# Optimization experiments

Measured on AMD Instinct MI355X. Metric: run time of the kernel, lower is better.

Reference implementation:

```python
import jax, jax.numpy as jnp
import numpy as np

B, L, H, E, F, C = 8, 8192, 512, 8, 1024, 2  # batch, seq, hidden, experts, ffn, capacity factor


def setup_inputs() -> dict:
    key = jax.random.key(0)
    ks = jax.random.split(key, 4)
    x = jax.random.normal(ks[0], (B, L, H), jnp.float32)
    Wg = jax.random.normal(ks[1], (H, E), jnp.float32) * (H ** -0.5)   # gate (no bias)
    W1 = jax.random.normal(ks[2], (E, H, F), jnp.float32) * (H ** -0.5)
    b1 = jnp.zeros((E, F), jnp.float32)
    W2 = jax.random.normal(ks[3], (E, F, H), jnp.float32) * (F ** -0.5)
    b2 = jnp.zeros((E, H), jnp.float32)
    return {"x": x, "Wg": Wg, "W1": W1, "b1": b1, "W2": W2, "b2": b2}


def reference(x, Wg, W1, b1, W2, b2):
    b, l, h = x.shape
    e = Wg.shape[1]
    k = min(max(int(l * C / e), 1), l)  # expert-choice capacity per expert
    # Gate scores: softmax over experts per token, then each expert picks its top-k tokens.
    S = jax.nn.softmax(x @ Wg, axis=-1)          # (b, l, E)
    St = jnp.swapaxes(S, 1, 2)                   # (b, E, l)
    G, I = jax.lax.top_k(St, k)                  # (b, E, k) scores / token indices
    # Dispatch: gather each expert's chosen tokens.
    ex = jnp.take_along_axis(x[:, None], I[..., None], axis=2)   # (b, E, k, h)
    # Grouped expert MLP (Linear -> GELU -> Linear), batched over experts.
    hmid = jax.nn.gelu(jnp.einsum('bekh,ehf->bekf', ex, W1) + b1[None, :, None, :],
                       approximate=False)
    out = jnp.einsum('bekf,efh->bekh', hmid, W2) + b2[None, :, None, :]
    vals = G[..., None] * out                    # weight by gate score
    # Combine: scatter-add expert outputs back to token positions.
    new_x = jnp.zeros_like(x).at[jnp.arange(b)[:, None, None], I].add(vals)
    return new_x
```

## Files before the change

kernel.cpp:

```cpp
#include <hip/hip_runtime.h>
#include <hip/hip_bf16.h>
#include <hip/hip_fp16.h>

typedef float f32x4 __attribute__((ext_vector_type(4)));
typedef _Float16 f16x8 __attribute__((ext_vector_type(8)));
typedef unsigned int u32x4 __attribute__((ext_vector_type(4)));

static constexpr int Bb = 8, Ll = 8192, Hh = 512, Ee = 8, Ff = 1024, KK = 2048;

static __device__ __forceinline__ float fast_rcp(float x) {
#if __has_builtin(__builtin_amdgcn_rcpf)
  return __builtin_amdgcn_rcpf(x);
#else
  return 1.0f / x;
#endif
}

static __device__ __forceinline__ float gelu_exact(float v) {
  float a = __builtin_fabsf(v) * 0.70710678118654752f;
  float t = fast_rcp(__builtin_fmaf(0.47047f, a, 1.0f));
  float p = __builtin_fmaf(0.7478556f, t, -0.0958798f);
  p = __builtin_fmaf(p, t, 0.3480242f);
  p = p * t;
  float e = __expf(-a * a);
  float er = __builtin_fmaf(-p, e, 1.0f);
  er = __builtin_copysignf(er, v);
  return 0.5f * v * (1.0f + er);
}

static __device__ __forceinline__ void nt_store16(const f16x8& v, _Float16* p) {
  __builtin_nontemporal_store(*reinterpret_cast<const u32x4*>(&v),
                              reinterpret_cast<u32x4*>(p));
}

__global__ __launch_bounds__(256) void transpose_cvt_kernel(const float* __restrict__ src,
                                                            _Float16* __restrict__ dst,
                                                            int R, int C) {
  __shared__ float tile[32][33];
  int z = blockIdx.z;
  const float* s = src + (size_t)z * R * C;
  _Float16* d = dst + (size_t)z * R * C;
  int c0 = blockIdx.x * 32, r0 = blockIdx.y * 32;
  int tx = threadIdx.x, ty = threadIdx.y;
#pragma unroll
  for (int i = ty; i < 32; i += 8) tile[i][tx] = s[(size_t)(r0 + i) * C + (c0 + tx)];
  __syncthreads();
#pragma unroll
  for (int i = ty; i < 32; i += 8) d[(size_t)(c0 + i) * R + (r0 + tx)] = (_Float16)tile[tx][i];
}

__global__ __launch_bounds__(256) void gatecvt_kernel(const float* __restrict__ x,
                                                      const float* __restrict__ Wg,
                                                      double* __restrict__ St,
                                                      _Float16* __restrict__ xb) {
  __shared__ float wgt[8][516];
  __shared__ float xs[32][132];
  int tid = threadIdx.x;
  for (int i = tid; i < Hh * Ee; i += 256) wgt[i & 7][i >> 3] = Wg[i];
  int row = tid >> 3, seg = tid & 7;
  int token0 = blockIdx.x * 32;
  const float* xrow = x + (size_t)(token0 + row) * Hh;
  _Float16* xbrow = xb + (size_t)(token0 + row) * Hh;
  float4 r0 = reinterpret_cast<const float4*>(xrow)[seg * 4 + 0];
  float4 r1 = reinterpret_cast<const float4*>(xrow)[seg * 4 + 1];
  float4 r2 = reinterpret_cast<const float4*>(xrow)[seg * 4 + 2];
  float4 r3 = reinterpret_cast<const float4*>(xrow)[seg * 4 + 3];
  double a0 = 0.0, a1 = 0.0, a2 = 0.0, a3 = 0.0;
  for (int c = 0; c < 4; ++c) {
    f16x8 h0, h1;
    h0[0] = (_Float16)r0.x; h0[1] = (_Float16)r0.y; h0[2] = (_Float16)r0.z; h0[3] = (_Float16)r0.w;
    h0[4] = (_Float16)r1.x; h0[5] = (_Float16)r1.y; h0[6] = (_Float16)r1.z; h0[7] = (_Float16)r1.w;
    h1[0] = (_Float16)r2.x; h1[1] = (_Float16)r2.y; h1[2] = (_Float16)r2.z; h1[3] = (_Float16)r2.w;
    h1[4] = (_Float16)r3.x; h1[5] = (_Float16)r3.y; h1[6] = (_Float16)r3.z; h1[7] = (_Float16)r3.w;
    nt_store16(h0, xbrow + c * 128 + seg * 16);
    nt_store16(h1, xbrow + c * 128 + seg * 16 + 8);
    __syncthreads();
    *reinterpret_cast<float4*>(&xs[row][seg * 16 + 0]) = r0;
    *reinterpret_cast<float4*>(&xs[row][seg * 16 + 4]) = r1;
    *reinterpret_cast<float4*>(&xs[row][seg * 16 + 8]) = r2;
    *reinterpret_cast<float4*>(&xs[row][seg * 16 + 12]) = r3;
    if (c + 1 < 4) {
      const float4* nx = reinterpret_cast<const float4*>(xrow + (c + 1) * 128);
      r0 = nx[seg * 4 + 0]; r1 = nx[seg * 4 + 1]; r2 = nx[seg * 4 + 2]; r3 = nx[seg * 4 + 3];
    }
    __syncthreads();
#pragma unroll
    for (int hh = 0; hh < 128; hh += 4) {
      float4 xv = *reinterpret_cast<const float4*>(&xs[row][hh]);
      float4 wv = *reinterpret_cast<const float4*>(&wgt[seg][c * 128 + hh]);
      a0 += (double)xv.x * (double)wv.x;
      a1 += (double)xv.y * (double)wv.y;
      a2 += (double)xv.z * (double)wv.z;
      a3 += (double)xv.w * (double)wv.w;
    }
  }
  double acc = (a0 + a1) + (a2 + a3);
  double m = acc;
  m = fmax(m, __shfl_xor(m, 1, 64));
  m = fmax(m, __shfl_xor(m, 2, 64));
  m = fmax(m, __shfl_xor(m, 4, 64));
  double ex = exp(acc - m);
  double s = ex;
  s += __shfl_xor(s, 1, 64);
  s += __shfl_xor(s, 2, 64);
  s += __shfl_xor(s, 4, 64);
  int token = token0 + row;
  int b = token >> 13, l = token & (Ll - 1);
  St[((size_t)(b * Ee + seg)) * Ll + l] = ex / s;
}

__global__ __launch_bounds__(1024) void topk_kernel(const double* __restrict__ St,
                                                    int* __restrict__ idx,
                                                    float* __restrict__ gate) {
  __shared__ unsigned long long keys[Ll];
  __shared__ unsigned int hist[256];
  __shared__ unsigned int sc[1024];
  __shared__ unsigned long long s_prefix;
  __shared__ int s_remaining;
  __shared__ unsigned long long redA[16], redO[16];
  int row = blockIdx.x;
  int tid = threadIdx.x;
  const double* s = St + (size_t)row * Ll;
  unsigned long long myA = ~0ULL, myO = 0ULL;
  for (int i = tid; i < Ll; i += 1024) {
    unsigned long long kx = (unsigned long long)__double_as_longlong(s[i]);
    keys[i] = kx;
    myA &= kx;
    myO |= kx;
  }
#pragma unroll
  for (int off2 = 32; off2 >= 1; off2 >>= 1) {
    myA &= __shfl_xor(myA, off2, 64);
    myO |= __shfl_xor(myO, off2, 64);
  }
  if ((tid & 63) == 0) { redA[tid >> 6] = myA; redO[tid >> 6] = myO; }
  __syncthreads();
  unsigned long long allA = redA[0], allO = redO[0];
#pragma unroll
  for (int w = 1; w < 16; ++w) { allA &= redA[w]; allO |= redO[w]; }
  unsigned long long diff = allA ^ allO;

  unsigned long long T;
  int nEqTake;
  if (diff == 0) {
    T = allA;
    nEqTake = KK;
  } else {
    int hb = 63 - __builtin_clzll(diff);
    int pv = hb >> 3;
    unsigned long long prefmask = (pv >= 7) ? 0ULL : (~0ULL << ((pv + 1) * 8));
    unsigned long long prefix = allA & prefmask;
    int remaining = KK;
    for (int p = pv; p >= 0; --p) {
      if (tid < 256) hist[tid] = 0;
      __syncthreads();
      int sh = p * 8;
      for (int i = tid; i < Ll; i += 1024) {
        unsigned long long kk = keys[i];
        if ((kk & prefmask) == prefix) atomicAdd(&hist[(unsigned)(kk >> sh) & 255u], 1u);
      }
      __syncthreads();
      if (tid < 256) sc[tid] = hist[tid];
      __syncthreads();
#pragma unroll
      for (int off = 1; off < 256; off <<= 1) {
        unsigned v = (tid < 256 && tid + off < 256) ? sc[tid + off] : 0;
        __syncthreads();
        if (tid < 256) sc[tid] += v;
        __syncthreads();
      }
      if (tid < 256) {
        unsigned incl = sc[tid];
        unsigned above = (tid == 255) ? 0u : sc[tid + 1];
        if ((int)incl >= remaining && (int)above < remaining) {
          s_remaining = remaining - (int)above;
          s_prefix = prefix | ((unsigned long long)(unsigned)tid << sh);
        }
      }
      __syncthreads();
      remaining = s_remaining;
      prefix = s_prefix;
      prefmask |= (255ULL << sh);
      __syncthreads();
    }
    T = prefix;
    nEqTake = remaining;
  }

  int base = tid * 8;
  unsigned long long kk[8];
  unsigned gtc = 0, eqc = 0;
#pragma unroll
  for (int j = 0; j < 8; ++j) {
    kk[j] = keys[base + j];
    gtc += (kk[j] > T);
    eqc += (kk[j] == T);
  }
  unsigned packed = (gtc << 16) | eqc;
  sc[tid] = packed;
  __syncthreads();
  for (int off = 1; off < 1024; off <<= 1) {
    unsigned v = (tid >= off) ? sc[tid - off] : 0;
    __syncthreads();
    sc[tid] += v;
    __syncthreads();
  }
  unsigned excl = sc[tid] - packed;
  int gtb = (int)(excl >> 16), eqb = (int)(excl & 0xFFFFu);
  int orow = row * KK;
#pragma unroll
  for (int j = 0; j < 8; ++j) {
    bool isgt = kk[j] > T, iseq = kk[j] == T;
    bool take = isgt || (iseq && eqb < nEqTake);
    if (take) {
      int pos = gtb + (eqb < nEqTake ? eqb : nEqTake);
      idx[orow + pos] = base + j;
      gate[orow + pos] = (float)__longlong_as_double((long long)kk[j]);
    }
    gtb += isgt ? 1 : 0;
    eqb += iseq ? 1 : 0;
  }
}

__global__ __launch_bounds__(256) void buildinv_kernel(const int* __restrict__ idx,
                                                       int* __restrict__ cnt,
                                                       int* __restrict__ inv) {
  int s = blockIdx.x * 256 + threadIdx.x;
  int gp = s >> 11;
  int b = gp >> 3;
  int t = idx[s];
  int key = b * Ll + t;
  int pos = atomicAdd(&cnt[key], 1);
  inv[key * 8 + pos] = s;
}

__global__ __launch_bounds__(256) void combine_kernel(const _Float16* __restrict__ yout,
                                                      const int* __restrict__ cnt,
                                                      const int* __restrict__ inv,
                                                      float* __restrict__ out) {
  int tglob = blockIdx.x * 4 + (threadIdx.x >> 6);
  int lane = threadIdx.x & 63;
  int n = cnt[tglob];
  float acc[8];
#pragma unroll
  for (int j = 0; j < 8; ++j) acc[j] = 0.f;
  for (int c = 0; c < n; ++c) {
    int s = inv[tglob * 8 + c];
    u32x4 u = __builtin_nontemporal_load(
        reinterpret_cast<const u32x4*>(yout + (size_t)s * Hh + lane * 8));
    f16x8 v = *reinterpret_cast<f16x8*>(&u);
#pragma unroll
    for (int j = 0; j < 8; ++j) acc[j] += (float)v[j];
  }
  float* o = out + (size_t)tglob * Hh + lane * 8;
  f32x4 lo = {acc[0], acc[1], acc[2], acc[3]};
  f32x4 hi = {acc[4], acc[5], acc[6], acc[7]};
  __builtin_nontemporal_store(lo, reinterpret_cast<f32x4*>(o));
  __builtin_nontemporal_store(hi, reinterpret_cast<f32x4*>(o + 4));
}

__global__ __launch_bounds__(512, 2) void gemm1_kernel(const _Float16* __restrict__ xb,
                                                       const _Float16* __restrict__ w1t,
                                                       const float* __restrict__ b1,
                                                       const int* __restrict__ idx,
                                                       _Float16* __restrict__ hmid,
                                                       int chunk_base) {
  __shared__ __align__(16) _Float16 lds[65536];
  int tid = threadIdx.x, lane = tid & 63, wid = tid >> 6;
  int nat = blockIdx.x;
  int rr = nat >> 8;
  int j = nat & 7;
  int idxb = (nat >> 3) & 31;
  int pl = rr * 8 + j;
  int bx = idxb & 3, by = idxb >> 2;
  int gp = chunk_base + pl;
  int b = gp >> 3, e = gp & 7;
  int m0 = by * 256, f0 = bx * 256;

  const _Float16* srcbase[4];
  int dstoff[4];
#pragma unroll
  for (int i = 0; i < 4; ++i) {
    int c = wid * 4 + i;
    int lr = (c & 15) * 16 + (lane >> 2);
    int q = lane & 3;
    int qg = q ^ ((lr >> 1) & 3);
    if (c < 16) {
      int token = idx[(size_t)gp * KK + m0 + lr];
      srcbase[i] = xb + ((size_t)b * Ll + token) * Hh + qg * 8;
      dstoff[i] = (c & 15) * 512;
    } else {
      srcbase[i] = w1t + ((size_t)e * Ff + f0 + lr) * Hh + qg * 8;
      dstoff[i] = 8192 + (c & 15) * 512;
    }
  }

  f32x4 acc[8][4] = {};
  int wm = wid >> 2, wn = wid & 3;
  int a_off[8], b_off[4];
  int ko = lane >> 4;
#pragma unroll
  for (int i = 0; i < 8; ++i) {
    int ra = wm * 128 + i * 16 + (lane & 15);
    a_off[i] = ra * 32 + (ko ^ ((ra >> 1) & 3)) * 8;
  }
#pragma unroll
  for (int i = 0; i < 4; ++i) {
    int rb = wn * 64 + i * 16 + (lane & 15);
    b_off[i] = 8192 + rb * 32 + (ko ^ ((rb >> 1) & 3)) * 8;
  }

  auto stage = [&](int p, int kt) {
#pragma unroll
    for (int i = 0; i < 4; ++i) {
      __builtin_amdgcn_global_load_lds(
          (const __attribute__((address_space(1))) void*)(srcbase[i] + kt),
          (__attribute__((address_space(3))) void*)(lds + p * 16384 + dstoff[i]), 16, 0, 0);
    }
  };

  constexpr int nt = Hh / 32;
  stage(0, 0);
  stage(1, 32);
  int cur = 0;
  for (int t = 0; t < nt; ++t) {
    __builtin_amdgcn_sched_barrier(0);
    if (t + 1 < nt) asm volatile("s_waitcnt vmcnt(4) lgkmcnt(0)" ::: "memory");
    else            asm volatile("s_waitcnt vmcnt(0) lgkmcnt(0)" ::: "memory");
    __builtin_amdgcn_s_barrier();
    __builtin_amdgcn_sched_barrier(0);
    if (t + 2 < nt) stage(cur == 0 ? 2 : cur - 1, (t + 2) * 32);
    const _Float16* buf = lds + cur * 16384;
    f16x8 af[8], bf[4];
#pragma unroll
    for (int i = 0; i < 8; ++i) af[i] = *reinterpret_cast<const f16x8*>(buf + a_off[i]);
#pragma unroll
    for (int i = 0; i < 4; ++i) bf[i] = *reinterpret_cast<const f16x8*>(buf + b_off[i]);
    __builtin_amdgcn_s_setprio(1);
#pragma unroll
    for (int fr = 0; fr < 8; ++fr)
#pragma unroll
      for (int fc = 0; fc < 4; ++fc)
        acc[fr][fc] = __builtin_amdgcn_mfma_f32_16x16x32_f16(af[fr], bf[fc], acc[fr][fc], 0, 0, 0);
    __builtin_amdgcn_s_setprio(0);
    cur = (cur == 2) ? 0 : cur + 1;
  }
  __syncthreads();

  int cidx = lane & 15, rbase = (lane >> 4) * 4;
  float b1v[4];
#pragma unroll
  for (int fc = 0; fc < 4; ++fc) b1v[fc] = b1[e * Ff + f0 + wn * 64 + fc * 16 + cidx];
#pragma unroll
  for (int fr = 0; fr < 8; ++fr) {
#pragma unroll
    for (int fc = 0; fc < 4; ++fc) {
#pragma unroll
      for (int r = 0; r < 4; ++r) {
        int lm = wm * 128 + fr * 16 + rbase + r;
        int lf = wn * 64 + fc * 16 + cidx;
        float v = acc[fr][fc][r] + b1v[fc];
        lds[lm * 256 + (((lf >> 3) ^ (lm & 7)) << 3) + (lf & 7)] = (_Float16)gelu_exact(v);
      }
    }
  }
  __syncthreads();
  _Float16* hd = hmid + (size_t)pl * KK * Ff;
  int orow = tid >> 5, seg = tid & 31;
#pragma unroll
  for (int pp = 0; pp < 16; ++pp) {
    int lm = pp * 16 + orow;
    f16x8 v = *reinterpret_cast<const f16x8*>(lds + lm * 256 + ((seg ^ (lm & 7)) << 3));
    nt_store16(v, hd + (size_t)(m0 + lm) * Ff + f0 + seg * 8);
  }
}

__global__ __launch_bounds__(512, 2) void gemm2_kernel(const _Float16* __restrict__ hmid,
                                                       const _Float16* __restrict__ w2t,
                                                       const float* __restrict__ b2,
                                                       const int* __restrict__ idx,
                                                       const float* __restrict__ gate,
                                                       _Float16* __restrict__ yout,
                                                       int chunk_base, int small8) {
  __shared__ __align__(16) _Float16 lds[65536];
  int tid = threadIdx.x, lane = tid & 63, wid = tid >> 6;
  int nat = blockIdx.x;
  int ci, by;
  if (small8) {
    int j = nat & 7;
    int idxb = nat >> 3;
    ci = j * 2 + (idxb >> 3);
    by = idxb & 7;
  } else {
    int rr = nat >> 8;
    int low = nat & 255;
    int j = low & 7;
    int idxb = low >> 3;
    ci = rr * 32 + j * 4 + (idxb >> 3);
    by = idxb & 7;
  }
  int pl = ci >> 1;
  int h0 = (ci & 1) * 256;
  int gp = chunk_base + pl;
  int e = gp & 7;
  int m0 = by * 256;

  const _Float16* srcbase[8];
  int dstoff[8];
#pragma unroll
  for (int i = 0; i < 8; ++i) {
    int c = wid * 8 + i;
    int lr = (c & 31) * 8 + (lane >> 3);
    int q = lane & 7;
    int qg = q ^ (lr & 7);
    if (c < 32) {
      srcbase[i] = hmid + ((size_t)pl * KK + m0 + lr) * Ff + qg * 8;
      dstoff[i] = (c & 31) * 512;
    } else {
      srcbase[i] = w2t + ((size_t)e * Hh + h0 + lr) * Ff + qg * 8;
      dstoff[i] = 16384 + (c & 31) * 512;
    }
  }

  f32x4 acc[8][4] = {};
  int wm = wid >> 2, wn = wid & 3;
  int a_off[8], b_off[4];
  int ko = lane >> 4;
#pragma unroll
  for (int i = 0; i < 8; ++i) {
    int ra = wm * 128 + i * 16 + (lane & 15);
    a_off[i] = ra * 64 + (ko ^ (ra & 7)) * 8;
  }
#pragma unroll
  for (int i = 0; i < 4; ++i) {
    int rb = wn * 64 + i * 16 + (lane & 15);
    b_off[i] = 16384 + rb * 64 + (ko ^ (rb & 7)) * 8;
  }

  auto stage = [&](int p, int kt) {
#pragma unroll
    for (int i = 0; i < 8; ++i) {
      __builtin_amdgcn_global_load_lds(
          (const __attribute__((address_space(1))) void*)(srcbase[i] + kt),
          (__attribute__((address_space(3))) void*)(lds + p * 32768 + dstoff[i]), 16, 0, 0);
    }
  };

  constexpr int nt = Ff / 64;
  stage(0, 0);
  for (int t = 0; t < nt; ++t) {
    __syncthreads();
    if (t + 1 < nt) stage((t + 1) & 1, (t + 1) * 64);
    const _Float16* buf = lds + (t & 1) * 32768;
#pragma unroll
    for (int half = 0; half < 2; ++half) {
      int kx = half * 32;
      f16x8 af[8], bf[4];
#pragma unroll
      for (int i = 0; i < 8; ++i) af[i] = *reinterpret_cast<const f16x8*>(buf + (a_off[i] ^ kx));
#pragma unroll
      for (int i = 0; i < 4; ++i) bf[i] = *reinterpret_cast<const f16x8*>(buf + (b_off[i] ^ kx));
      __builtin_amdgcn_s_setprio(1);
#pragma unroll
      for (int fr = 0; fr < 8; ++fr)
#pragma unroll
        for (int fc = 0; fc < 4; ++fc)
          acc[fr][fc] = __builtin_amdgcn_mfma_f32_16x16x32_f16(af[fr], bf[fc], acc[fr][fc], 0, 0, 0);
      __builtin_amdgcn_s_setprio(0);
    }
  }
  __syncthreads();

  int cidx = lane & 15, rbase = (lane >> 4) * 4;
  float b2v[4];
#pragma unroll
  for (int fc = 0; fc < 4; ++fc) b2v[fc] = b2[e * Hh + h0 + wn * 64 + fc * 16 + cidx];
#pragma unroll
  for (int fr = 0; fr < 8; ++fr) {
    float gv[4];
#pragma unroll
    for (int r = 0; r < 4; ++r) {
      int lm = wm * 128 + fr * 16 + rbase + r;
      gv[r] = gate[(size_t)gp * KK + m0 + lm];
    }
#pragma unroll
    for (int fc = 0; fc < 4; ++fc) {
#pragma unroll
      for (int r = 0; r < 4; ++r) {
        int lm = wm * 128 + fr * 16 + rbase + r;
        int lh = wn * 64 + fc * 16 + cidx;
        float v = acc[fr][fc][r] + b2v[fc];
        lds[lm * 256 + (((lh >> 3) ^ (lm & 7)) << 3) + (lh & 7)] = (_Float16)(gv[r] * v);
      }
    }
  }
  __syncthreads();
  int orow = tid >> 5, seg = tid & 31;
#pragma unroll
  for (int pp = 0; pp < 16; ++pp) {
    int lm = pp * 16 + orow;
    f16x8 v = *reinterpret_cast<const f16x8*>(lds + lm * 256 + ((seg ^ (lm & 7)) << 3));
    nt_store16(v, yout + ((size_t)gp * KK + m0 + lm) * Hh + h0 + seg * 8);
  }
}

extern "C" void kernel_launch(void* const* d_in, const int* in_sizes, int n_in,
                              void* d_out, int out_size, void* d_ws, size_t ws_size,
                              hipStream_t stream) {
  const float* x  = (const float*)d_in[0];
  const float* Wg = (const float*)d_in[1];
  const float* W1 = (const float*)d_in[2];
  const float* b1 = (const float*)d_in[3];
  const float* W2 = (const float*)d_in[4];
  const float* b2 = (const float*)d_in[5];
  float* out = (float*)d_out;

  char* ws = (char*)d_ws;
  size_t off = 0;
  auto alloc = [&](size_t bytes) -> char* {
    char* p = ws + off;
    off = (off + bytes + 255) & ~(size_t)255;
    return p;
  };
  _Float16* xb   = (_Float16*)alloc((size_t)Bb * Ll * Hh * 2);
  _Float16* w1t  = (_Float16*)alloc((size_t)Ee * Ff * Hh * 2);
  _Float16* w2t  = (_Float16*)alloc((size_t)Ee * Hh * Ff * 2);
  double*   St   = (double*)alloc((size_t)Bb * Ee * Ll * 8);
  int*      dI   = (int*)alloc((size_t)Bb * Ee * KK * 4);
  float*    dG   = (float*)alloc((size_t)Bb * Ee * KK * 4);
  int*      cnt  = (int*)alloc((size_t)Bb * Ll * 4);
  int*      inv  = (int*)alloc((size_t)Bb * Ll * 8 * 4);
  _Float16* yout = (_Float16*)alloc((size_t)Bb * Ee * KK * Hh * 2);
  size_t fixed = off;
  size_t per_pair = (size_t)KK * Ff * 2;
  int chunk = 8;
  if (fixed + per_pair * 32 <= ws_size) chunk = 32;
  else if (fixed + per_pair * 16 <= ws_size) chunk = 16;
  _Float16* hmid = (_Float16*)alloc(per_pair * (size_t)chunk);

  hipMemsetAsync(cnt, 0, (size_t)Bb * Ll * 4, stream);
  gatecvt_kernel<<<Bb * Ll / 32, 256, 0, stream>>>(x, Wg, St, xb);
  transpose_cvt_kernel<<<dim3(Ff / 32, Hh / 32, Ee), dim3(32, 8), 0, stream>>>(W1, w1t, Hh, Ff);
  transpose_cvt_kernel<<<dim3(Hh / 32, Ff / 32, Ee), dim3(32, 8), 0, stream>>>(W2, w2t, Ff, Hh);
  topk_kernel<<<Bb * Ee, 1024, 0, stream>>>(St, dI, dG);
  buildinv_kernel<<<Bb * Ee * KK / 256, 256, 0, stream>>>(dI, cnt, inv);

  for (int cb = 0; cb < Bb * Ee; cb += chunk) {
    gemm1_kernel<<<chunk * 32, 512, 0, stream>>>(xb, w1t, b1, dI, hmid, cb);
    gemm2_kernel<<<chunk * 16, 512, 0, stream>>>(hmid, w2t, b2, dI, dG, yout, cb,
                                                 chunk == 8 ? 1 : 0);
  }
  combine_kernel<<<Bb * Ll / 4, 256, 0, stream>>>(yout, cnt, inv, out);
}
```

Before: 529.4 us.

## Shrink GEMM tiles to 128x256 with 256-thread blocks and simpler double buffering

```diff
diff --git a/kernel.cpp b/kernel.cpp
--- a/kernel.cpp
+++ b/kernel.cpp
@@ -259,78 +259,75 @@
   __builtin_nontemporal_store(hi, reinterpret_cast<f32x4*>(o + 4));
 }
 
-__global__ __launch_bounds__(512, 2) void gemm1_kernel(const _Float16* __restrict__ xb,
+__global__ __launch_bounds__(256, 2) void gemm1_kernel(const _Float16* __restrict__ xb,
                                                        const _Float16* __restrict__ w1t,
                                                        const float* __restrict__ b1,
                                                        const int* __restrict__ idx,
                                                        _Float16* __restrict__ hmid,
                                                        int chunk_base) {
-  __shared__ __align__(16) _Float16 lds[65536];
+  __shared__ __align__(16) _Float16 lds[32768];
   int tid = threadIdx.x, lane = tid & 63, wid = tid >> 6;
   int nat = blockIdx.x;
-  int rr = nat >> 8;
   int j = nat & 7;
-  int idxb = (nat >> 3) & 31;
-  int pl = rr * 8 + j;
+  int m = nat >> 3;
+  int pp = m >> 6;
+  int idxb = m & 63;
+  int pl = pp * 8 + j;
   int bx = idxb & 3, by = idxb >> 2;
   int gp = chunk_base + pl;
   int b = gp >> 3, e = gp & 7;
-  int m0 = by * 256, f0 = bx * 256;
-
-  const _Float16* srcbase[4];
-  int dstoff[4];
-#pragma unroll
-  for (int i = 0; i < 4; ++i) {
-    int c = wid * 4 + i;
-    int lr = (c & 15) * 16 + (lane >> 2);
+  int m0 = by * 128, f0 = bx * 256;
+
+  const _Float16* srcbase[6];
+  int dstoff[6];
+#pragma unroll
+  for (int i = 0; i < 6; ++i) {
+    int c = wid * 6 + i;
     int q = lane & 3;
-    int qg = q ^ ((lr >> 1) & 3);
-    if (c < 16) {
+    if (c < 8) {
+      int lr = c * 16 + (lane >> 2);
+      int qg = q ^ ((lr >> 1) & 3);
       int token = idx[(size_t)gp * KK + m0 + lr];
       srcbase[i] = xb + ((size_t)b * Ll + token) * Hh + qg * 8;
-      dstoff[i] = (c & 15) * 512;
+      dstoff[i] = c * 512;
     } else {
+      int cb = c - 8;
+      int lr = cb * 16 + (lane >> 2);
+      int qg = q ^ ((lr >> 1) & 3);
       srcbase[i] = w1t + ((size_t)e * Ff + f0 + lr) * Hh + qg * 8;
-      dstoff[i] = 8192 + (c & 15) * 512;
+      dstoff[i] = 4096 + cb * 512;
     }
   }
 
   f32x4 acc[8][4] = {};
-  int wm = wid >> 2, wn = wid & 3;
   int a_off[8], b_off[4];
   int ko = lane >> 4;
 #pragma unroll
   for (int i = 0; i < 8; ++i) {
-    int ra = wm * 128 + i * 16 + (lane & 15);
+    int ra = i * 16 + (lane & 15);
     a_off[i] = ra * 32 + (ko ^ ((ra >> 1) & 3)) * 8;
   }
 #pragma unroll
   for (int i = 0; i < 4; ++i) {
-    int rb = wn * 64 + i * 16 + (lane & 15);
-    b_off[i] = 8192 + rb * 32 + (ko ^ ((rb >> 1) & 3)) * 8;
+    int rb = wid * 64 + i * 16 + (lane & 15);
+    b_off[i] = 4096 + rb * 32 + (ko ^ ((rb >> 1) & 3)) * 8;
   }
 
   auto stage = [&](int p, int kt) {
 #pragma unroll
-    for (int i = 0; i < 4; ++i) {
+    for (int i = 0; i < 6; ++i) {
       __builtin_amdgcn_global_load_lds(
           (const __attribute__((address_space(1))) void*)(srcbase[i] + kt),
-          (__attribute__((address_space(3))) void*)(lds + p * 16384 + dstoff[i]), 16, 0, 0);
+          (__attribute__((address_space(3))) void*)(lds + p * 12288 + dstoff[i]), 16, 0, 0);
     }
   };
 
   constexpr int nt = Hh / 32;
   stage(0, 0);
-  stage(1, 32);
-  int cur = 0;
   for (int t = 0; t < nt; ++t) {
-    __builtin_amdgcn_sched_barrier(0);
-    if (t + 1 < nt) asm volatile("s_waitcnt vmcnt(4) lgkmcnt(0)" ::: "memory");
-    else            asm volatile("s_waitcnt vmcnt(0) lgkmcnt(0)" ::: "memory");
-    __builtin_amdgcn_s_barrier();
-    __builtin_amdgcn_sched_barrier(0);
-    if (t + 2 < nt) stage(cur == 0 ? 2 : cur - 1, (t + 2) * 32);
-    const _Float16* buf = lds + cur * 16384;
+    __syncthreads();
+    if (t + 1 < nt) stage((t + 1) & 1, (t + 1) * 32);
+    const _Float16* buf = lds + (t & 1) * 12288;
     f16x8 af[8], bf[4];
 #pragma unroll
     for (int i = 0; i < 8; ++i) af[i] = *reinterpret_cast<const f16x8*>(buf + a_off[i]);
@@ -343,22 +340,21 @@
       for (int fc = 0; fc < 4; ++fc)
         acc[fr][fc] = __builtin_amdgcn_mfma_f32_16x16x32_f16(af[fr], bf[fc], acc[fr][fc], 0, 0, 0);
     __builtin_amdgcn_s_setprio(0);
-    cur = (cur == 2) ? 0 : cur + 1;
   }
   __syncthreads();
 
   int cidx = lane & 15, rbase = (lane >> 4) * 4;
   float b1v[4];
 #pragma unroll
-  for (int fc = 0; fc < 4; ++fc) b1v[fc] = b1[e * Ff + f0 + wn * 64 + fc * 16 + cidx];
+  for (int fc = 0; fc < 4; ++fc) b1v[fc] = b1[e * Ff + f0 + wid * 64 + fc * 16 + cidx];
 #pragma unroll
   for (int fr = 0; fr < 8; ++fr) {
 #pragma unroll
     for (int fc = 0; fc < 4; ++fc) {
 #pragma unroll
       for (int r = 0; r < 4; ++r) {
-        int lm = wm * 128 + fr * 16 + rbase + r;
-        int lf = wn * 64 + fc * 16 + cidx;
+        int lm = fr * 16 + rbase + r;
+        int lf = wid * 64 + fc * 16 + cidx;
         float v = acc[fr][fc][r] + b1v[fc];
         lds[lm * 256 + (((lf >> 3) ^ (lm & 7)) << 3) + (lf & 7)] = (_Float16)gelu_exact(v);
       }
@@ -368,127 +364,115 @@
   _Float16* hd = hmid + (size_t)pl * KK * Ff;
   int orow = tid >> 5, seg = tid & 31;
 #pragma unroll
-  for (int pp = 0; pp < 16; ++pp) {
-    int lm = pp * 16 + orow;
+  for (int q = 0; q < 16; ++q) {
+    int lm = q * 8 + orow;
     f16x8 v = *reinterpret_cast<const f16x8*>(lds + lm * 256 + ((seg ^ (lm & 7)) << 3));
     nt_store16(v, hd + (size_t)(m0 + lm) * Ff + f0 + seg * 8);
   }
 }
 
-__global__ __launch_bounds__(512, 2) void gemm2_kernel(const _Float16* __restrict__ hmid,
+__global__ __launch_bounds__(256, 2) void gemm2_kernel(const _Float16* __restrict__ hmid,
                                                        const _Float16* __restrict__ w2t,
                                                        const float* __restrict__ b2,
                                                        const int* __restrict__ idx,
                                                        const float* __restrict__ gate,
                                                        _Float16* __restrict__ yout,
-                                                       int chunk_base, int small8) {
-  __shared__ __align__(16) _Float16 lds[65536];
+                                                       int chunk_base) {
+  __shared__ __align__(16) _Float16 lds[32768];
   int tid = threadIdx.x, lane = tid & 63, wid = tid >> 6;
   int nat = blockIdx.x;
-  int ci, by;
-  if (small8) {
-    int j = nat & 7;
-    int idxb = nat >> 3;
-    ci = j * 2 + (idxb >> 3);
-    by = idxb & 7;
-  } else {
-    int rr = nat >> 8;
-    int low = nat & 255;
-    int j = low & 7;
-    int idxb = low >> 3;
-    ci = rr * 32 + j * 4 + (idxb >> 3);
-    by = idxb & 7;
-  }
-  int pl = ci >> 1;
-  int h0 = (ci & 1) * 256;
+  int j = nat & 7;
+  int m = nat >> 3;
+  int pp = m >> 5;
+  int idxb = m & 31;
+  int pl = pp * 8 + j;
+  int bx = idxb & 1, by = idxb >> 1;
   int gp = chunk_base + pl;
   int e = gp & 7;
-  int m0 = by * 256;
-
-  const _Float16* srcbase[8];
-  int dstoff[8];
-#pragma unroll
-  for (int i = 0; i < 8; ++i) {
-    int c = wid * 8 + i;
-    int lr = (c & 31) * 8 + (lane >> 3);
-    int q = lane & 7;
-    int qg = q ^ (lr & 7);
-    if (c < 32) {
+  int m0 = by * 128, h0 = bx * 256;
+
+  const _Float16* srcbase[6];
+  int dstoff[6];
+#pragma unroll
+  for (int i = 0; i < 6; ++i) {
+    int c = wid * 6 + i;
+    int q = lane & 3;
+    if (c < 8) {
+      int lr = c * 16 + (lane >> 2);
+      int qg = q ^ ((lr >> 1) & 3);
       srcbase[i] = hmid + ((size_t)pl * KK + m0 + lr) * Ff + qg * 8;
-      dstoff[i] = (c & 31) * 512;
+      dstoff[i] = c * 512;
     } else {
+      int cb = c - 8;
+      int lr = cb * 16 + (lane >> 2);
+      int qg = q ^ ((lr >> 1) & 3);
       srcbase[i] = w2t + ((size_t)e * Hh + h0 + lr) * Ff + qg * 8;
-      dstoff[i] = 16384 + (c & 31) * 512;
+      dstoff[i] = 4096 + cb * 512;
     }
   }
 
   f32x4 acc[8][4] = {};
-  int wm = wid >> 2, wn = wid & 3;
   int a_off[8], b_off[4];
   int ko = lane >> 4;
 #pragma unroll
   for (int i = 0; i < 8; ++i) {
-    int ra = wm * 128 + i * 16 + (lane & 15);
-    a_off[i] = ra * 64 + (ko ^ (ra & 7)) * 8;
+    int ra = i * 16 + (lane & 15);
+    a_off[i] = ra * 32 + (ko ^ ((ra >> 1) & 3)) * 8;
   }
 #pragma unroll
   for (int i = 0; i < 4; ++i) {
-    int rb = wn * 64 + i * 16 + (lane & 15);
-    b_off[i] = 16384 + rb * 64 + (ko ^ (rb & 7)) * 8;
+    int rb = wid * 64 + i * 16 + (lane & 15);
+    b_off[i] = 4096 + rb * 32 + (ko ^ ((rb >> 1) & 3)) * 8;
   }
 
   auto stage = [&](int p, int kt) {
 #pragma unroll
-    for (int i = 0; i < 8; ++i) {
+    for (int i = 0; i < 6; ++i) {
       __builtin_amdgcn_global_load_lds(
           (const __attribute__((address_space(1))) void*)(srcbase[i] + kt),
-          (__attribute__((address_space(3))) void*)(lds + p * 32768 + dstoff[i]), 16, 0, 0);
+          (__attribute__((address_space(3))) void*)(lds + p * 12288 + dstoff[i]), 16, 0, 0);
     }
   };
 
-  constexpr int nt = Ff / 64;
+  constexpr int nt = Ff / 32;
   stage(0, 0);
   for (int t = 0; t < nt; ++t) {
     __syncthreads();
-    if (t + 1 < nt) stage((t + 1) & 1, (t + 1) * 64);
-    const _Float16* buf = lds + (t & 1) * 32768;
-#pragma unroll
-    for (int half = 0; half < 2; ++half) {
-      int kx = half * 32;
-      f16x8 af[8], bf[4];
-#pragma unroll
-      for (int i = 0; i < 8; ++i) af[i] = *reinterpret_cast<const f16x8*>(buf + (a_off[i] ^ kx));
-#pragma unroll
-      for (int i = 0; i < 4; ++i) bf[i] = *reinterpret_cast<const f16x8*>(buf + (b_off[i] ^ kx));
-      __builtin_amdgcn_s_setprio(1);
-#pragma unroll
-      for (int fr = 0; fr < 8; ++fr)
-#pragma unroll
-        for (int fc = 0; fc < 4; ++fc)
-          acc[fr][fc] = __builtin_amdgcn_mfma_f32_16x16x32_f16(af[fr], bf[fc], acc[fr][fc], 0, 0, 0);
-      __builtin_amdgcn_s_setprio(0);
-    }
+    if (t + 1 < nt) stage((t + 1) & 1, (t + 1) * 32);
+    const _Float16* buf = lds + (t & 1) * 12288;
+    f16x8 af[8], bf[4];
+#pragma unroll
+    for (int i = 0; i < 8; ++i) af[i] = *reinterpret_cast<const f16x8*>(buf + a_off[i]);
+#pragma unroll
+    for (int i = 0; i < 4; ++i) bf[i] = *reinterpret_cast<const f16x8*>(buf + b_off[i]);
+    __builtin_amdgcn_s_setprio(1);
+#pragma unroll
+    for (int fr = 0; fr < 8; ++fr)
+#pragma unroll
+      for (int fc = 0; fc < 4; ++fc)
+        acc[fr][fc] = __builtin_amdgcn_mfma_f32_16x16x32_f16(af[fr], bf[fc], acc[fr][fc], 0, 0, 0);
+    __builtin_amdgcn_s_setprio(0);
   }
   __syncthreads();
 
   int cidx = lane & 15, rbase = (lane >> 4) * 4;
   float b2v[4];
 #pragma unroll
-  for (int fc = 0; fc < 4; ++fc) b2v[fc] = b2[e * Hh + h0 + wn * 64 + fc * 16 + cidx];
+  for (int fc = 0; fc < 4; ++fc) b2v[fc] = b2[e * Hh + h0 + wid * 64 + fc * 16 + cidx];
 #pragma unroll
   for (int fr = 0; fr < 8; ++fr) {
     float gv[4];
 #pragma unroll
     for (int r = 0; r < 4; ++r) {
-      int lm = wm * 128 + fr * 16 + rbase + r;
+      int lm = fr * 16 + rbase + r;
       gv[r] = gate[(size_t)gp * KK + m0 + lm];
     }
 #pragma unroll
     for (int fc = 0; fc < 4; ++fc) {
 #pragma unroll
       for (int r = 0; r < 4; ++r) {
-        int lm = wm * 128 + fr * 16 + rbase + r;
-        int lh = wn * 64 + fc * 16 + cidx;
+        int lm = fr * 16 + rbase + r;
+        int lh = wid * 64 + fc * 16 + cidx;
         float v = acc[fr][fc][r] + b2v[fc];
         lds[lm * 256 + (((lh >> 3) ^ (lm & 7)) << 3) + (lh & 7)] = (_Float16)(gv[r] * v);
       }
@@ -497,8 +481,8 @@
   __syncthreads();
   int orow = tid >> 5, seg = tid & 31;
 #pragma unroll
-  for (int pp = 0; pp < 16; ++pp) {
-    int lm = pp * 16 + orow;
+  for (int q = 0; q < 16; ++q) {
+    int lm = q * 8 + orow;
     f16x8 v = *reinterpret_cast<const f16x8*>(lds + lm * 256 + ((seg ^ (lm & 7)) << 3));
     nt_store16(v, yout + ((size_t)gp * KK + m0 + lm) * Hh + h0 + seg * 8);
   }
@@ -546,9 +530,8 @@
   buildinv_kernel<<<Bb * Ee * KK / 256, 256, 0, stream>>>(dI, cnt, inv);
 
   for (int cb = 0; cb < Bb * Ee; cb += chunk) {
-    gemm1_kernel<<<chunk * 32, 512, 0, stream>>>(xb, w1t, b1, dI, hmid, cb);
-    gemm2_kernel<<<chunk * 16, 512, 0, stream>>>(hmid, w2t, b2, dI, dG, yout, cb,
-                                                 chunk == 8 ? 1 : 0);
+    gemm1_kernel<<<chunk * 64, 256, 0, stream>>>(xb, w1t, b1, dI, hmid, cb);
+    gemm2_kernel<<<chunk * 32, 256, 0, stream>>>(hmid, w2t, b2, dI, dG, yout, cb);
   }
   combine_kernel<<<Bb * Ll / 4, 256, 0, stream>>>(yout, cnt, inv, out);
 }
```

New measurement: 540.1 us. +2.0%, slower.
